# Kernel optimization log

Hardware: AMD Instinct MI355X
Metric: run time of the kernel (lower is better)

Reference implementation:

```python
import jax, jax.numpy as jnp
import numpy as np

jax.config.update("jax_enable_x64", True)  # original torch code runs in float64; minors underflow fp32

D = 96   # Nsites
N = 48   # Nparticles


def setup_inputs() -> dict:
    key = jax.random.key(0)
    # Orthonormal single-particle orbitals (columns), as the module assumes (P^T P = I)
    A = jax.random.normal(key, (D, D), dtype=jnp.float64)
    Q, _ = jnp.linalg.qr(A)
    P = Q[:, :N]  # [D, N]
    # A valid ordered particle configuration: strictly increasing, occ_positions[k] <= D-N+k
    occ_positions = jnp.arange(N, dtype=jnp.int32) * (D // N)  # stride-2 filling
    return {"P": P, "occ_positions": occ_positions}


def _cond_probs(P, occ_positions):
    """Conditional probabilities probs[k, x] of placing the k-th (ordered) particle at
    site x given particles 0..k-1 at occ_positions[0..k-1].

    Math identical to SlaterDetSampler_ordered.get_cond_prob (naive_update=True):
      G = I - P P^T
      probs[k,x] = -det(M_x[0:x+1,0:x+1]) / det(M[0:xmin,0:xmin])
    where M = G - diag(occupancy of particles < k) and M_x additionally sets n_x = 1.
    Since Ksites is always the contiguous range 0..x, all determinants are LEADING
    principal minors; and because only the (x,x) diagonal entry changes by -1 (last index
    of the block), det(M_x block) = d_{x+1} - d_x with d_j the leading j-minor of M.
    """
    Dd, Nn = P.shape
    dt = P.dtype
    eye = jnp.eye(Dd, dtype=dt)
    G = eye - P @ P.T                                             # [D, D]

    onehots = jax.nn.one_hot(occ_positions, Dd, dtype=dt)         # [N, D]
    n_before = jnp.cumsum(onehots, axis=0) - onehots              # occupancy of particles < k
    A = G[None] - n_before[:, :, None] * eye                      # [N, D, D]: G - diag(n_<k)

    # All leading principal minors via batched det of masked matrices:
    # M_j = A on the [0:j,0:j] block, identity elsewhere  =>  det(M_j) = leading j-minor
    ii = jnp.arange(Dd)
    jj = jnp.arange(1, Dd + 1)
    blk = (ii[None, :, None] < jj[:, None, None]) & (ii[None, None, :] < jj[:, None, None])  # [D,D,D]
    Ms = jnp.where(blk[None], A[:, None], eye)                    # [N, D, D, D]
    d = jnp.linalg.det(Ms.reshape(Nn * Dd, Dd, Dd)).reshape(Nn, Dd)
    d_full = jnp.concatenate([jnp.ones((Nn, 1), dt), d], axis=1)  # d_full[k, j] = j-th leading minor

    k = jnp.arange(Nn)
    xmin = jnp.where(k == 0, 0, occ_positions[jnp.maximum(k - 1, 0)] + 1)  # [N]
    xmax = Dd - Nn + k + 1                                                  # [N]
    denom = jnp.take_along_axis(d_full, xmin[:, None], axis=1)              # [N, 1]
    num = d_full[:, 1:] - d_full[:, :-1]                                    # det(GG_num) per candidate x

    x = jnp.arange(Dd)
    support = (x[None, :] >= xmin[:, None]) & (x[None, :] < xmax[:, None])
    probs = jnp.where(support, -num / denom, jnp.zeros((), dt))
    # torch.where(abs(probs) > 1e-15, probs, 0.)
    probs = jnp.where(jnp.abs(probs) > 1e-15, probs, jnp.zeros((), dt))
    return probs


def reference(P, occ_positions):
    probs = _cond_probs(P, occ_positions)                          # [N, D]
    # prob of the full ordered sample = prod_k probs[k, occ_positions[k]]  (as in sample())
    p_k = jnp.take_along_axis(probs, occ_positions[:, None], axis=1)[:, 0]
    prob_sample = jnp.prod(p_k)
    return probs, prob_sample
```

## Files before the change

kernel.cpp:

```cpp
#include <hip/hip_runtime.h>
#include <math.h>

#define Dd 96
#define Nn 48
#define LD 97
#define PTS 98

__device__ __forceinline__ double frcp(double x) {
    double r = __builtin_amdgcn_rcp(x);
    r = fma(fma(-x, r, 1.0), r, r);
    r = fma(fma(-x, r, 1.0), r, r);
    return r;
}

__attribute__((amdgpu_waves_per_eu(4, 4)))
__global__ __launch_bounds__(1024) void slater_kernel(const float* __restrict__ P,
                                                      const int* __restrict__ occ,
                                                      float* __restrict__ out,
                                                      unsigned* __restrict__ cnt) {
    __shared__ double As[Dd * LD];
    __shared__ double Sbuf[2][6][Dd];
    __shared__ double aBuf[2][Dd][8];
    __shared__ double ev[2][6];
    __shared__ int    evmask[2], sdead[2];
    __shared__ double evm[6];
    __shared__ int    evmmask;
    __shared__ double gs_runprod;
    __shared__ int    gs_dead;
    __shared__ unsigned char flag[Dd];
    float* PT = (float*)As;

    const int tid  = threadIdx.x;
    const int k    = blockIdx.x;
    const int n    = Dd - Nn + k + 1;
    const int lane = tid & 63;
    const int wave = tid >> 6;
    const int xmin = (k == 0) ? 0 : occ[k - 1] + 1;

    if (tid < Dd) flag[tid] = 0;
    __syncthreads();
    if (tid < k) flag[occ[tid]] = 1;
    for (int e = tid; e < Dd * Nn; e += 1024) {
        int c = e / Nn, t = e - (e / Nn) * Nn;
        PT[t * PTS + c] = P[e];
    }
    __syncthreads();

    double Areg[8]; int trs[2], tcs[2];
#pragma unroll
    for (int it = 0; it < 2; ++it) {
        int tau = tid + 1024 * it;
        double s00 = 0.0, s01 = 0.0, s10 = 0.0, s11 = 0.0;
        int tr = 0, tc = 0;
        if (tau < 1176) {
            tr = (int)((97.0 - sqrt(9409.0 - 8.0 * (double)tau)) * 0.5);
            while ((tr * (97 - tr)) / 2 > tau) --tr;
            while (((tr + 1) * (96 - tr)) / 2 <= tau) ++tr;
            tc = tr + (tau - (tr * (97 - tr)) / 2);
            int r0 = 2 * tr, c0 = 2 * tc;
            if (r0 < n && c0 < n) {
                for (int t = 0; t < Nn; ++t) {
                    const float* row = PT + t * PTS;
                    float2 pr = *(const float2*)(row + r0);
                    float2 pc = *(const float2*)(row + c0);
                    s00 -= (double)pr.x * (double)pc.x; s01 -= (double)pr.x * (double)pc.y;
                    s10 -= (double)pr.y * (double)pc.x; s11 -= (double)pr.y * (double)pc.y;
                }
            }
        }
        trs[it] = tr; tcs[it] = tc;
        Areg[it * 4 + 0] = s00; Areg[it * 4 + 1] = s01;
        Areg[it * 4 + 2] = s10; Areg[it * 4 + 3] = s11;
    }
    __syncthreads();
#pragma unroll
    for (int it = 0; it < 2; ++it) {
        int tau = tid + 1024 * it;
        if (tau < 1176) {
            int tr = trs[it], tc = tcs[it];
            int r0 = 2 * tr, c0 = 2 * tc;
            if (r0 < n && c0 < n) {
                bool r1 = (r0 + 1 < n), c1 = (c0 + 1 < n);
                double d0 = flag[r0] ? 0.0 : 1.0;
                double d1 = flag[r0 + 1] ? 0.0 : 1.0;
                As[r0 * LD + c0] = Areg[it * 4 + 0] + ((r0 == c0) ? d0 : 0.0);
                if (c1)       As[r0 * LD + c0 + 1]       = Areg[it * 4 + 1];
                if (r1)       As[(r0 + 1) * LD + c0]     = Areg[it * 4 + 2];
                if (r1 && c1) As[(r0 + 1) * LD + c0 + 1] = Areg[it * 4 + 3] + ((r0 == c0) ? d1 : 0.0);
                if (tr != tc) {
                    As[c0 * LD + r0] = Areg[it * 4 + 0];
                    if (c1)       As[(c0 + 1) * LD + r0]     = Areg[it * 4 + 1];
                    if (r1)       As[c0 * LD + r0 + 1]       = Areg[it * 4 + 2];
                    if (r1 && c1) As[(c0 + 1) * LD + r0 + 1] = Areg[it * 4 + 3];
                }
            }
        }
    }
    __syncthreads();

    double myprob = 0.0;
    double rr[6][2];

    auto prefactor = [&](int jb, int p, double grun, int gdead) {
        double Bd[6][6];
#pragma unroll
        for (int u = 0; u < 6; ++u)
#pragma unroll
            for (int r = 0; r < 6; ++r)
                Bd[u][r] = __shfl((r & 1) ? rr[u][1] : rr[u][0], (jb + r) >> 1, 64);
        int msk = 0;
#pragma unroll
        for (int cc = 0; cc < 6; ++cc) {
            double piv = Bd[cc][cc];
            double ap = fabs(piv);
            int jj = jb + cc;
            if (!gdead) {
                if (jj >= xmin) {
                    if (lane == 0) ev[p][cc] = grun * (1.0 - piv);
                    msk |= (1 << cc);
                    double nr = grun * piv;
                    if (!(ap > 1e-7) || !(ap < 8.0) || !(fabs(nr) > 1e-8)) gdead = 1;
                    else grun = nr;
                } else {
                    if (!(ap > 1e-12) || !(ap < 8.0)) gdead = 1;
                }
            }
            double rp = frcp(piv);
            Bd[cc][cc] = rp;
#pragma unroll
            for (int i = cc + 1; i < 6; ++i) {
                double m = Bd[i][cc] * rp;
                Bd[i][cc] = m;
#pragma unroll
                for (int r = cc + 1; r < 6; ++r) Bd[i][r] -= m * Bd[cc][r];
            }
        }
        if (lane == 0) {
            evmask[p] = msk; sdead[p] = gdead;
            gs_runprod = grun; gs_dead = gdead;
        }
        if (lane < 48) {
            const bool live = (2 * lane >= jb + 6);
#pragma unroll
            for (int sl = 0; sl < 2; ++sl) {
                double s0 = rr[0][sl];
                double s1 = rr[1][sl] - Bd[1][0] * s0;
                double s2 = rr[2][sl] - Bd[2][0] * s0 - Bd[2][1] * s1;
                double s3 = rr[3][sl] - Bd[3][0] * s0 - Bd[3][1] * s1 - Bd[3][2] * s2;
                double s4 = rr[4][sl] - Bd[4][0] * s0 - Bd[4][1] * s1 - Bd[4][2] * s2 - Bd[4][3] * s3;
                double s5 = rr[5][sl] - Bd[5][0] * s0 - Bd[5][1] * s1 - Bd[5][2] * s2 - Bd[5][3] * s3 - Bd[5][4] * s4;
                s5 = s5 * Bd[5][5];
                s4 = (s4 - Bd[4][5] * s5) * Bd[4][4];
                s3 = (s3 - Bd[3][4] * s4 - Bd[3][5] * s5) * Bd[3][3];
                s2 = (s2 - Bd[2][3] * s3 - Bd[2][4] * s4 - Bd[2][5] * s5) * Bd[2][2];
                s1 = (s1 - Bd[1][2] * s2 - Bd[1][3] * s3 - Bd[1][4] * s4 - Bd[1][5] * s5) * Bd[1][1];
                s0 = (s0 - Bd[0][1] * s1 - Bd[0][2] * s2 - Bd[0][3] * s3 - Bd[0][4] * s4 - Bd[0][5] * s5) * Bd[0][0];
                Sbuf[p][0][2 * lane + sl] = live ? s0 : 0.0;
                Sbuf[p][1][2 * lane + sl] = live ? s1 : 0.0;
                Sbuf[p][2][2 * lane + sl] = live ? s2 : 0.0;
                Sbuf[p][3][2 * lane + sl] = live ? s3 : 0.0;
                Sbuf[p][4][2 * lane + sl] = live ? s4 : 0.0;
                Sbuf[p][5][2 * lane + sl] = live ? s5 : 0.0;
            }
        }
    };

#pragma unroll
    for (int u = 0; u < 6; ++u) {
        if (lane < 48) {
            rr[u][0] = As[(6 * wave + u) * LD + 2 * lane];
            rr[u][1] = As[(6 * wave + u) * LD + 2 * lane + 1];
        } else { rr[u][0] = 0.0; rr[u][1] = 0.0; }
    }
    if (wave >= 1 && lane < 3) {
#pragma unroll
        for (int u = 0; u < 6; ++u) {
            aBuf[0][6 * wave + u][2 * lane]     = rr[u][0];
            aBuf[0][6 * wave + u][2 * lane + 1] = rr[u][1];
        }
    }
    if (wave == 0) prefactor(0, 0, 1.0, 0);
    __syncthreads();

    int j = 0, s = 0;
    for (; j + 6 <= n - 1; j += 6, ++s) {
        const int par = s & 1;
        if (tid >= j && tid < j + 6) {
            int q = tid - j;
            if ((evmask[par] >> q) & 1) myprob = ev[par][q];
        }
        if (sdead[par]) break;
        const bool nexts = (j + 12 <= n - 1);

        if (wave >= s + 1) {
            if (lane < 48) {
                double S0[6], S1[6];
#pragma unroll
                for (int r = 0; r < 6; ++r) {
                    double2 sv = *(const double2*)&Sbuf[par][r][2 * lane];
                    S0[r] = sv.x; S1[r] = sv.y;
                }
#pragma unroll
                for (int u = 0; u < 6; ++u) {
                    const double* ab = &aBuf[par][6 * wave + u][0];
                    double2 q0 = *(const double2*)(ab + 0);
                    double2 q1 = *(const double2*)(ab + 2);
                    double2 q2 = *(const double2*)(ab + 4);
                    rr[u][0] -= q0.x * S0[0] + q0.y * S0[1] + q1.x * S0[2]
                              + q1.y * S0[3] + q2.x * S0[4] + q2.y * S0[5];
                    rr[u][1] -= q0.x * S1[0] + q0.y * S1[1] + q1.x * S1[2]
                              + q1.y * S1[3] + q2.x * S1[4] + q2.y * S1[5];
                }
                if (nexts && wave >= s + 2) {
                    int d = lane - 3 * (s + 1);
                    if (d >= 0 && d < 3) {
#pragma unroll
                        for (int u = 0; u < 6; ++u) {
                            aBuf[par ^ 1][6 * wave + u][2 * d]     = rr[u][0];
                            aBuf[par ^ 1][6 * wave + u][2 * d + 1] = rr[u][1];
                        }
                    }
                }
            }
            if (nexts && wave == s + 1)
                prefactor(j + 6, par ^ 1, gs_runprod, gs_dead);
        }
        __syncthreads();
    }

    const int  jend = j;
    const bool full = (jend + 6 > n - 1);
    if (full && wave == (jend / 6)) {
        const int rsz = n - jend;
        double Bm[6][6];
#pragma unroll
        for (int u = 0; u < 6; ++u)
#pragma unroll
            for (int r = 0; r < 6; ++r)
                Bm[u][r] = __shfl((r & 1) ? rr[u][1] : rr[u][0], (jend + r) >> 1, 64);
        if (lane == 0) {
            double grun = gs_runprod; int gdead = gs_dead;
            int msk = 0;
            double evs[6] = {0.0, 0.0, 0.0, 0.0, 0.0, 0.0};
            for (int q = 0; q < rsz - 1; ++q) {
                if (gdead) break;
                double piv = Bm[q][q];
                double ap = fabs(piv);
                int jj = jend + q;
                if (jj >= xmin) {
                    evs[q] = grun * (1.0 - piv); msk |= (1 << q);
                    double nr = grun * piv;
                    if (!(ap > 1e-7) || !(ap < 8.0) || !(fabs(nr) > 1e-8)) gdead = 1;
                    else grun = nr;
                } else {
                    if (!(ap > 1e-12) || !(ap < 8.0)) gdead = 1;
                }
                if (!gdead) {
                    double rp = frcp(piv);
                    for (int i = q + 1; i < rsz; ++i) {
                        double m = Bm[i][q] * rp;
                        for (int r = q + 1; r < rsz; ++r) Bm[i][r] -= m * Bm[q][r];
                    }
                }
            }
            if (!gdead) {
                evs[rsz - 1] = grun * (1.0 - Bm[rsz - 1][rsz - 1]);
                msk |= (1 << (rsz - 1));
            }
#pragma unroll
            for (int q = 0; q < 6; ++q) evm[q] = evs[q];
            evmmask = msk;
        }
    }
    __syncthreads();
    if (full && tid >= jend && tid < n) {
        int q = tid - jend;
        if ((evmmask >> q) & 1) myprob = evm[q];
    }

    if (tid < Dd) {
        double p = myprob;
        if (!isfinite(p)) p = 0.0;
        if (!(fabs(p) > 1e-15)) p = 0.0;
        p = fmin(fmax(p, 0.0), 1.0);
        out[k * Dd + tid] = (float)p;
    }

    __threadfence();
    __syncthreads();
    if (wave == 0) {
        int old = 0;
        if (lane == 0)
            old = (int)__hip_atomic_fetch_add(cnt, 1u, __ATOMIC_ACQ_REL,
                                              __HIP_MEMORY_SCOPE_AGENT);
        old = __shfl(old, 0, 64);
        if (((unsigned)old + 1u) % (unsigned)Nn == 0u) {
            __threadfence();
            double v = 1.0;
            if (lane < Nn) {
                float f = __hip_atomic_load(out + lane * Dd + occ[lane],
                                            __ATOMIC_RELAXED, __HIP_MEMORY_SCOPE_AGENT);
                v = (double)f;
            }
#pragma unroll
            for (int off = 32; off >= 1; off >>= 1)
                v *= __shfl_down(v, off, 64);
            if (lane == 0) {
                if (!isfinite(v)) v = 0.0;
                out[Nn * Dd] = (float)v;
            }
        }
    }
}

extern "C" void kernel_launch(void* const* d_in, const int* in_sizes, int n_in,
                              void* d_out, int out_size, void* d_ws, size_t ws_size,
                              hipStream_t stream) {
    const float* P = (const float*)d_in[0];
    const int* occ = (const int*)d_in[1];
    float* out = (float*)d_out;

    slater_kernel<<<Nn, 1024, 0, stream>>>(P, occ, out, (unsigned*)d_ws);
}
```

Baseline: 110.3 us.

## Replace shuffled LU block solve with in-register Gauss-Jordan via readlane broadcasts

The panel prefactor no longer gathers a 6x6 block through shuffles and runs a separate LU forward/back solve. It now does Gauss-Jordan elimination directly on the per-lane row registers, using scalar readlane broadcasts for the pivots and multipliers. The trailing update reads its coefficients by readlane from each wave's own registers instead of staging them in an LDS aBuf, which removes that buffer and its writes. The tail block is also handled across the whole wave instead of by one lane, and the launch hint changes from waves_per_eu to launch_bounds(1024,1). In exchange there are more dependent readlane instructions and redundant arithmetic on all lanes.

```diff
diff --git a/kernel.cpp b/kernel.cpp
--- a/kernel.cpp
+++ b/kernel.cpp
@@ -13,14 +13,20 @@
     return r;
 }
 
-__attribute__((amdgpu_waves_per_eu(4, 4)))
-__global__ __launch_bounds__(1024) void slater_kernel(const float* __restrict__ P,
-                                                      const int* __restrict__ occ,
-                                                      float* __restrict__ out,
-                                                      unsigned* __restrict__ cnt) {
+__device__ __forceinline__ double rdlane(double v, int srcLane) {
+    union { double d; int i[2]; } u; u.d = v;
+    int lo = __builtin_amdgcn_readlane(u.i[0], srcLane);
+    int hi = __builtin_amdgcn_readlane(u.i[1], srcLane);
+    union { int i[2]; double d; } w; w.i[0] = lo; w.i[1] = hi;
+    return w.d;
+}
+
+__global__ __launch_bounds__(1024, 1) void slater_kernel(const float* __restrict__ P,
+                                                         const int* __restrict__ occ,
+                                                         float* __restrict__ out,
+                                                         unsigned* __restrict__ cnt) {
     __shared__ double As[Dd * LD];
     __shared__ double Sbuf[2][6][Dd];
-    __shared__ double aBuf[2][Dd][8];
     __shared__ double ev[2][6];
     __shared__ int    evmask[2], sdead[2];
     __shared__ double evm[6];
@@ -102,19 +108,15 @@
     double rr[6][2];
 
     auto prefactor = [&](int jb, int p, double grun, int gdead) {
-        double Bd[6][6];
-#pragma unroll
-        for (int u = 0; u < 6; ++u)
-#pragma unroll
-            for (int r = 0; r < 6; ++r)
-                Bd[u][r] = __shfl((r & 1) ? rr[u][1] : rr[u][0], (jb + r) >> 1, 64);
+        const int jbH = jb >> 1;
         int msk = 0;
 #pragma unroll
         for (int cc = 0; cc < 6; ++cc) {
-            double piv = Bd[cc][cc];
-            double ap = fabs(piv);
-            int jj = jb + cc;
+            const int src = jbH + (cc >> 1);
+            double piv = rdlane(rr[cc][cc & 1], src);
             if (!gdead) {
+                double ap = fabs(piv);
+                int jj = jb + cc;
                 if (jj >= xmin) {
                     if (lane == 0) ev[p][cc] = grun * (1.0 - piv);
                     msk |= (1 << cc);
@@ -126,13 +128,13 @@
                 }
             }
             double rp = frcp(piv);
-            Bd[cc][cc] = rp;
-#pragma unroll
-            for (int i = cc + 1; i < 6; ++i) {
-                double m = Bd[i][cc] * rp;
-                Bd[i][cc] = m;
-#pragma unroll
-                for (int r = cc + 1; r < 6; ++r) Bd[i][r] -= m * Bd[cc][r];
+            rr[cc][0] *= rp; rr[cc][1] *= rp;
+#pragma unroll
+            for (int i = 0; i < 6; ++i) {
+                if (i == cc) continue;
+                double f = rdlane(rr[i][cc & 1], src);
+                rr[i][0] -= f * rr[cc][0];
+                rr[i][1] -= f * rr[cc][1];
             }
         }
         if (lane == 0) {
@@ -142,25 +144,9 @@
         if (lane < 48) {
             const bool live = (2 * lane >= jb + 6);
 #pragma unroll
-            for (int sl = 0; sl < 2; ++sl) {
-                double s0 = rr[0][sl];
-                double s1 = rr[1][sl] - Bd[1][0] * s0;
-                double s2 = rr[2][sl] - Bd[2][0] * s0 - Bd[2][1] * s1;
-                double s3 = rr[3][sl] - Bd[3][0] * s0 - Bd[3][1] * s1 - Bd[3][2] * s2;
-                double s4 = rr[4][sl] - Bd[4][0] * s0 - Bd[4][1] * s1 - Bd[4][2] * s2 - Bd[4][3] * s3;
-                double s5 = rr[5][sl] - Bd[5][0] * s0 - Bd[5][1] * s1 - Bd[5][2] * s2 - Bd[5][3] * s3 - Bd[5][4] * s4;
-                s5 = s5 * Bd[5][5];
-                s4 = (s4 - Bd[4][5] * s5) * Bd[4][4];
-                s3 = (s3 - Bd[3][4] * s4 - Bd[3][5] * s5) * Bd[3][3];
-                s2 = (s2 - Bd[2][3] * s3 - Bd[2][4] * s4 - Bd[2][5] * s5) * Bd[2][2];
-                s1 = (s1 - Bd[1][2] * s2 - Bd[1][3] * s3 - Bd[1][4] * s4 - Bd[1][5] * s5) * Bd[1][1];
-                s0 = (s0 - Bd[0][1] * s1 - Bd[0][2] * s2 - Bd[0][3] * s3 - Bd[0][4] * s4 - Bd[0][5] * s5) * Bd[0][0];
-                Sbuf[p][0][2 * lane + sl] = live ? s0 : 0.0;
-                Sbuf[p][1][2 * lane + sl] = live ? s1 : 0.0;
-                Sbuf[p][2][2 * lane + sl] = live ? s2 : 0.0;
-                Sbuf[p][3][2 * lane + sl] = live ? s3 : 0.0;
-                Sbuf[p][4][2 * lane + sl] = live ? s4 : 0.0;
-                Sbuf[p][5][2 * lane + sl] = live ? s5 : 0.0;
+            for (int r = 0; r < 6; ++r) {
+                Sbuf[p][r][2 * lane]     = live ? rr[r][0] : 0.0;
+                Sbuf[p][r][2 * lane + 1] = live ? rr[r][1] : 0.0;
             }
         }
     };
@@ -171,13 +157,6 @@
             rr[u][0] = As[(6 * wave + u) * LD + 2 * lane];
             rr[u][1] = As[(6 * wave + u) * LD + 2 * lane + 1];
         } else { rr[u][0] = 0.0; rr[u][1] = 0.0; }
-    }
-    if (wave >= 1 && lane < 3) {
-#pragma unroll
-        for (int u = 0; u < 6; ++u) {
-            aBuf[0][6 * wave + u][2 * lane]     = rr[u][0];
-            aBuf[0][6 * wave + u][2 * lane + 1] = rr[u][1];
-        }
     }
     if (wave == 0) prefactor(0, 0, 1.0, 0);
     __syncthreads();
@@ -192,39 +171,25 @@
         if (sdead[par]) break;
         const bool nexts = (j + 12 <= n - 1);
 
-        if (wave >= s + 1) {
-            if (lane < 48) {
-                double S0[6], S1[6];
+        if (wave >= s + 1 && lane < 48) {
+            double S0[6], S1[6];
+#pragma unroll
+            for (int r = 0; r < 6; ++r) {
+                double2 sv = *(const double2*)&Sbuf[par][r][2 * lane];
+                S0[r] = sv.x; S1[r] = sv.y;
+            }
+#pragma unroll
+            for (int u = 0; u < 6; ++u) {
 #pragma unroll
                 for (int r = 0; r < 6; ++r) {
-                    double2 sv = *(const double2*)&Sbuf[par][r][2 * lane];
-                    S0[r] = sv.x; S1[r] = sv.y;
-                }
-#pragma unroll
-                for (int u = 0; u < 6; ++u) {
-                    const double* ab = &aBuf[par][6 * wave + u][0];
-                    double2 q0 = *(const double2*)(ab + 0);
-                    double2 q1 = *(const double2*)(ab + 2);
-                    double2 q2 = *(const double2*)(ab + 4);
-                    rr[u][0] -= q0.x * S0[0] + q0.y * S0[1] + q1.x * S0[2]
-                              + q1.y * S0[3] + q2.x * S0[4] + q2.y * S0[5];
-                    rr[u][1] -= q0.x * S1[0] + q0.y * S1[1] + q1.x * S1[2]
-                              + q1.y * S1[3] + q2.x * S1[4] + q2.y * S1[5];
-                }
-                if (nexts && wave >= s + 2) {
-                    int d = lane - 3 * (s + 1);
-                    if (d >= 0 && d < 3) {
-#pragma unroll
-                        for (int u = 0; u < 6; ++u) {
-                            aBuf[par ^ 1][6 * wave + u][2 * d]     = rr[u][0];
-                            aBuf[par ^ 1][6 * wave + u][2 * d + 1] = rr[u][1];
-                        }
-                    }
-                }
-            }
-            if (nexts && wave == s + 1)
-                prefactor(j + 6, par ^ 1, gs_runprod, gs_dead);
-        }
+                    double a = rdlane(rr[u][r & 1], 3 * s + (r >> 1));
+                    rr[u][0] -= a * S0[r];
+                    rr[u][1] -= a * S1[r];
+                }
+            }
+        }
+        if (nexts && wave == s + 1)
+            prefactor(j + 6, par ^ 1, gs_runprod, gs_dead);
         __syncthreads();
     }
 
@@ -232,45 +197,42 @@
     const bool full = (jend + 6 > n - 1);
     if (full && wave == (jend / 6)) {
         const int rsz = n - jend;
-        double Bm[6][6];
-#pragma unroll
-        for (int u = 0; u < 6; ++u)
-#pragma unroll
-            for (int r = 0; r < 6; ++r)
-                Bm[u][r] = __shfl((r & 1) ? rr[u][1] : rr[u][0], (jend + r) >> 1, 64);
-        if (lane == 0) {
-            double grun = gs_runprod; int gdead = gs_dead;
-            int msk = 0;
-            double evs[6] = {0.0, 0.0, 0.0, 0.0, 0.0, 0.0};
-            for (int q = 0; q < rsz - 1; ++q) {
-                if (gdead) break;
-                double piv = Bm[q][q];
-                double ap = fabs(piv);
-                int jj = jend + q;
-                if (jj >= xmin) {
-                    evs[q] = grun * (1.0 - piv); msk |= (1 << q);
-                    double nr = grun * piv;
-                    if (!(ap > 1e-7) || !(ap < 8.0) || !(fabs(nr) > 1e-8)) gdead = 1;
-                    else grun = nr;
-                } else {
-                    if (!(ap > 1e-12) || !(ap < 8.0)) gdead = 1;
-                }
+        const int jeH = jend >> 1;
+        double grun = gs_runprod; int gdead = gs_dead;
+        int msk = 0;
+#pragma unroll
+        for (int cc = 0; cc < 6; ++cc) {
+            const int src = jeH + (cc >> 1);
+            double piv = rdlane(rr[cc][cc & 1], src);
+            double evv = 0.0;
+            if (cc < rsz - 1) {
                 if (!gdead) {
-                    double rp = frcp(piv);
-                    for (int i = q + 1; i < rsz; ++i) {
-                        double m = Bm[i][q] * rp;
-                        for (int r = q + 1; r < rsz; ++r) Bm[i][r] -= m * Bm[q][r];
+                    double ap = fabs(piv);
+                    int jj = jend + cc;
+                    if (jj >= xmin) {
+                        evv = grun * (1.0 - piv); msk |= (1 << cc);
+                        double nr = grun * piv;
+                        if (!(ap > 1e-7) || !(ap < 8.0) || !(fabs(nr) > 1e-8)) gdead = 1;
+                        else grun = nr;
+                    } else {
+                        if (!(ap > 1e-12) || !(ap < 8.0)) gdead = 1;
                     }
                 }
-            }
-            if (!gdead) {
-                evs[rsz - 1] = grun * (1.0 - Bm[rsz - 1][rsz - 1]);
-                msk |= (1 << (rsz - 1));
-            }
-#pragma unroll
-            for (int q = 0; q < 6; ++q) evm[q] = evs[q];
-            evmmask = msk;
-        }
+            } else if (cc == rsz - 1) {
+                if (!gdead) { evv = grun * (1.0 - piv); msk |= (1 << cc); }
+            }
+            if (lane == 0) evm[cc] = evv;
+            double rp = frcp(piv);
+            rr[cc][0] *= rp; rr[cc][1] *= rp;
+#pragma unroll
+            for (int i = 0; i < 6; ++i) {
+                if (i == cc) continue;
+                double f = rdlane(rr[i][cc & 1], src);
+                rr[i][0] -= f * rr[cc][0];
+                rr[i][1] -= f * rr[cc][1];
+            }
+        }
+        if (lane == 0) evmmask = msk;
     }
     __syncthreads();
     if (full && tid >= jend && tid < n) {
```

Result: faster. 97.73 us (-11.4%).
